# Optimization experiments

Hardware: AMD Instinct MI355X
Metric: run time of the kernel (lower is better)

## Reference

```python
import jax, jax.numpy as jnp
import numpy as np

VOCAB = 50257
EMBED = 256
NFREQ = 64
NRULES = 100
B, S = 4, 1024


def setup_inputs() -> dict:
    key = jax.random.key(0)
    ks = jax.random.split(key, 7)
    return {
        "token_ids": jax.random.randint(ks[0], (B, S), 0, VOCAB),
        "a_n": jax.random.normal(ks[1], (VOCAB, NFREQ), dtype=jnp.float32),
        "b_n": jax.random.normal(ks[2], (VOCAB, NFREQ), dtype=jnp.float32),
        "rule_transform": jax.random.normal(ks[3], (NRULES, EMBED, EMBED), dtype=jnp.float32),
        "token_rules": jax.random.randint(ks[4], (VOCAB,), 0, NRULES),
        "proj_w": jax.random.normal(ks[5], (EMBED, NFREQ), dtype=jnp.float32) * (1.0 / np.sqrt(NFREQ)),
        "proj_b": jax.random.normal(ks[6], (EMBED,), dtype=jnp.float32) * 0.01,
    }


def reference(token_ids, a_n, b_n, rule_transform, token_rules, proj_w, proj_b):
    vocab_size, nfreq = a_n.shape
    # fourier_freqs = linspace(1, F, F) -> [1..F]
    freqs = jnp.arange(1, nfreq + 1, dtype=jnp.float32)  # [F]
    x = token_ids.astype(jnp.float32)[..., None] / vocab_size  # [B,S,1]
    ang = (2.0 * jnp.pi) * freqs * x  # [B,S,F]
    # gather per-token fourier coefficients, fuse cos/sin combine
    fourier = a_n[token_ids] * jnp.cos(ang) + b_n[token_ids] * jnp.sin(ang)  # [B,S,F]
    base = jnp.einsum('bsf,df->bsd', fourier, proj_w) + proj_b  # [B,S,D]
    rule_idx = token_rules[token_ids]  # [B,S]
    rules = rule_transform[rule_idx]  # [B,S,D,D] gathered per token
    return jnp.einsum('bsd,bsde->bse', base, rules)  # [B,S,D]
```

## Files before the change

kernel.cpp:

```cpp
#include <hip/hip_runtime.h>
#include <math.h>

#define VOCAB   50257
#define EMBED   256
#define NFREQ   64
#define NRULES  100
#define NTOK    4096
#define CAP     256
#define CHUNK   16
#define NCHUNK  (CAP / CHUNK)

#define BASE_BYTES ((size_t)NTOK * EMBED * 4)
#define LIST_BYTES ((size_t)NRULES * CAP * 4)

__global__ __launch_bounds__(256) void prep_kernel(
    const float* __restrict__ proj_w,
    float*       __restrict__ wT,
    int*         __restrict__ counts)
{
    __shared__ float s_t[64 * 65];
    const int tid = threadIdx.x;
    const int b   = blockIdx.x;

    if (b == 0 && tid < NRULES) counts[tid] = 0;

    const float4* __restrict__ W4 =
        (const float4*)(proj_w + (size_t)b * 64 * NFREQ);
    #pragma unroll
    for (int i = 0; i < 4; ++i) {
        const int v = i * 256 + tid;
        const float4 w = W4[v];
        const int dl = v >> 4, f0 = (v & 15) * 4;
        s_t[dl * 65 + f0 + 0] = w.x;
        s_t[dl * 65 + f0 + 1] = w.y;
        s_t[dl * 65 + f0 + 2] = w.z;
        s_t[dl * 65 + f0 + 3] = w.w;
    }
    __syncthreads();
    #pragma unroll
    for (int j = 0; j < 16; ++j) {
        const int o = j * 256 + tid;
        const int f = o >> 6, c = o & 63;
        wT[f * EMBED + b * 64 + c] = s_t[c * 65 + f];
    }
}

__global__ __launch_bounds__(256) void fused_base_kernel(
    const int*   __restrict__ token_ids,
    const float* __restrict__ a_n,
    const float* __restrict__ b_n,
    const int*   __restrict__ token_rules,
    const float* __restrict__ wT,
    const float* __restrict__ proj_b,
    float*       __restrict__ base,
    int*         __restrict__ counts,
    int*         __restrict__ list)
{
    __shared__ float s_four[4][NFREQ];

    const int tid = threadIdx.x;
    const int tl  = tid >> 6;
    const int f   = tid & 63;
    const int tok_idx = blockIdx.x * 4 + tl;
    const int tok     = token_ids[tok_idx];

    const float x = (float)tok / (float)VOCAB;
    float sv, cv;
    sincosf(6.283185307179586f * x * (float)(f + 1), &sv, &cv);
    s_four[tl][f] = a_n[(size_t)tok * NFREQ + f] * cv
                  + b_n[(size_t)tok * NFREQ + f] * sv;

    if (f == 0) {
        const int rule = token_rules[tok];
        const int pos  = atomicAdd(&counts[rule], 1);
        if (pos < CAP) list[rule * CAP + pos] = tok_idx;
    }
    __syncthreads();

    const int   d    = tid;
    const float bias = proj_b[d];
    float a0 = bias, a1 = bias, a2 = bias, a3 = bias;

    #pragma unroll 4
    for (int q = 0; q < 16; ++q) {
        const float w0 = wT[(4 * q + 0) * EMBED + d];
        const float w1 = wT[(4 * q + 1) * EMBED + d];
        const float w2 = wT[(4 * q + 2) * EMBED + d];
        const float w3 = wT[(4 * q + 3) * EMBED + d];
        const float4 f0 = ((const float4*)s_four[0])[q];
        const float4 f1 = ((const float4*)s_four[1])[q];
        const float4 f2 = ((const float4*)s_four[2])[q];
        const float4 f3 = ((const float4*)s_four[3])[q];
        a0 += w0 * f0.x + w1 * f0.y + w2 * f0.z + w3 * f0.w;
        a1 += w0 * f1.x + w1 * f1.y + w2 * f1.z + w3 * f1.w;
        a2 += w0 * f2.x + w1 * f2.y + w2 * f2.z + w3 * f2.w;
        a3 += w0 * f3.x + w1 * f3.y + w2 * f3.z + w3 * f3.w;
    }
    base[(size_t)(blockIdx.x * 4 + 0) * EMBED + d] = a0;
    base[(size_t)(blockIdx.x * 4 + 1) * EMBED + d] = a1;
    base[(size_t)(blockIdx.x * 4 + 2) * EMBED + d] = a2;
    base[(size_t)(blockIdx.x * 4 + 3) * EMBED + d] = a3;
}

__global__ __launch_bounds__(512) void apply_kernel(
    const float* __restrict__ base,
    const float* __restrict__ rule_transform,
    const int*   __restrict__ counts,
    const int*   __restrict__ list,
    float*       __restrict__ out)
{
    __shared__ float s_mem[8192];

    const int rule = blockIdx.x;
    int cnt = counts[rule];
    if (cnt > CAP) cnt = CAP;
    const int t0 = blockIdx.y * CHUNK;
    if (t0 >= cnt) return;

    const int tid  = threadIdx.x;
    const int w8   = tid >> 6;
    const int ds   = w8 >> 1;
    const int eh   = w8 & 1;
    const int lane = tid & 63;

    #pragma unroll
    for (int i = 0; i < 8; ++i) {
        const int el = i * 512 + tid;
        int tt = t0 + (el >> 8);
        if (tt > cnt - 1) tt = cnt - 1;
        const int row = list[rule * CAP + tt];
        s_mem[el] = base[(size_t)row * EMBED + (el & 255)];
    }
    __syncthreads();

    const float2* __restrict__ T2 =
        (const float2*)(rule_transform + (size_t)rule * EMBED * EMBED);
    const int d0 = ds * 64;
    const int ec = eh * 64 + lane;

    float2 acc[CHUNK];
    #pragma unroll
    for (int t = 0; t < CHUNK; ++t) { acc[t].x = 0.f; acc[t].y = 0.f; }

    float2 tv[4], tvn[4];
    #pragma unroll
    for (int i = 0; i < 4; ++i)
        tv[i] = T2[(size_t)(d0 + i) * 128 + ec];

    for (int dq = 0; dq < 16; ++dq) {
        if (dq < 15) {
            #pragma unroll
            for (int i = 0; i < 4; ++i)
                tvn[i] = T2[(size_t)(d0 + dq * 4 + 4 + i) * 128 + ec];
        }
        #pragma unroll
        for (int t = 0; t < CHUNK; ++t) {
            const float4 b4 = *(const float4*)&s_mem[t * EMBED + d0 + dq * 4];
            acc[t].x += b4.x * tv[0].x + b4.y * tv[1].x + b4.z * tv[2].x + b4.w * tv[3].x;
            acc[t].y += b4.x * tv[0].y + b4.y * tv[1].y + b4.z * tv[2].y + b4.w * tv[3].y;
        }
        #pragma unroll
        for (int i = 0; i < 4; ++i) tv[i] = tvn[i];
    }

    __syncthreads();
    if (ds == 1 || ds == 3) {
        float2* dst = (float2*)(s_mem + ((ds >> 1) * 2 + eh) * 2048);
        #pragma unroll
        for (int t = 0; t < CHUNK; ++t) dst[t * 64 + lane] = acc[t];
    }
    __syncthreads();
    if (ds == 0 || ds == 2) {
        const float2* src = (const float2*)(s_mem + ((ds >> 1) * 2 + eh) * 2048);
        #pragma unroll
        for (int t = 0; t < CHUNK; ++t) {
            const float2 r = src[t * 64 + lane];
            acc[t].x += r.x; acc[t].y += r.y;
        }
    }
    __syncthreads();
    if (ds == 2) {
        float2* dst = (float2*)(s_mem + eh * 2048);
        #pragma unroll
        for (int t = 0; t < CHUNK; ++t) dst[t * 64 + lane] = acc[t];
    }
    __syncthreads();
    if (ds == 0) {
        const float2* src = (const float2*)(s_mem + eh * 2048);
        #pragma unroll
        for (int t = 0; t < CHUNK; ++t) {
            const float2 r = src[t * 64 + lane];
            acc[t].x += r.x; acc[t].y += r.y;
        }
        #pragma unroll
        for (int t = 0; t < CHUNK; ++t) {
            if (t0 + t < cnt) {
                const int row = list[rule * CAP + t0 + t];
                *(float2*)&out[(size_t)row * EMBED + eh * 128 + lane * 2] = acc[t];
            }
        }
    }
}

extern "C" void kernel_launch(void* const* d_in, const int* in_sizes, int n_in,
                              void* d_out, int out_size, void* d_ws, size_t ws_size,
                              hipStream_t stream) {
    const int*   token_ids      = (const int*)  d_in[0];
    const float* a_n            = (const float*)d_in[1];
    const float* b_n            = (const float*)d_in[2];
    const float* rule_transform = (const float*)d_in[3];
    const int*   token_rules    = (const int*)  d_in[4];
    const float* proj_w         = (const float*)d_in[5];
    const float* proj_b         = (const float*)d_in[6];
    float*       out            = (float*)d_out;

    float* base   = (float*)d_ws;
    int*   counts = (int*)((char*)d_ws + BASE_BYTES);
    int*   list   = (int*)((char*)d_ws + BASE_BYTES + 512);
    float* wT     = (float*)((char*)d_ws + BASE_BYTES + 512 + LIST_BYTES);

    prep_kernel<<<4, 256, 0, stream>>>(proj_w, wT, counts);
    fused_base_kernel<<<NTOK / 4, 256, 0, stream>>>(
        token_ids, a_n, b_n, token_rules, wT, proj_b, base, counts, list);
    apply_kernel<<<dim3(NRULES, NCHUNK), 512, 0, stream>>>(
        base, rule_transform, counts, list, out);
}
```

Before: 127.9 us.

## Tile apply kernel over output columns and loop over token tiles per rule

The apply kernel now splits each rule's work by output column tiles (64 columns per block, 4 blocks per rule) instead of by 16-token chunks, and each block loops over all of that rule's tokens in tiles of 48. Each thread covers the full 256-long reduction for one output column, so the cross-wave shared-memory reduction and its barriers are gone. Each rule matrix slice is now read once per token tile rather than once per 16-token chunk, which cuts rule_transform traffic. The trade-off is fewer blocks (400, all resident) with a serial loop over token tiles, a longer per-thread dependency chain, and less parallelism for rules with few tokens.

```diff
diff --git a/kernel.cpp b/kernel.cpp
--- a/kernel.cpp
+++ b/kernel.cpp
@@ -7,8 +7,9 @@
 #define NRULES  100
 #define NTOK    4096
 #define CAP     256
-#define CHUNK   16
-#define NCHUNK  (CAP / CHUNK)
+#define ETILE   64
+#define TTILE   48
+#define TPG     (TTILE / 4)
 
 #define BASE_BYTES ((size_t)NTOK * EMBED * 4)
 #define LIST_BYTES ((size_t)NRULES * CAP * 4)
@@ -102,101 +103,72 @@
     base[(size_t)(blockIdx.x * 4 + 3) * EMBED + d] = a3;
 }
 
-__global__ __launch_bounds__(512) void apply_kernel(
+__global__ __launch_bounds__(256) void apply_kernel(
     const float* __restrict__ base,
     const float* __restrict__ rule_transform,
     const int*   __restrict__ counts,
     const int*   __restrict__ list,
     float*       __restrict__ out)
 {
-    __shared__ float s_mem[8192];
+    __shared__ float s_base[TTILE * EMBED];
 
     const int rule = blockIdx.x;
     int cnt = counts[rule];
     if (cnt > CAP) cnt = CAP;
-    const int t0 = blockIdx.y * CHUNK;
-    if (t0 >= cnt) return;
+    if (cnt <= 0) return;
 
-    const int tid  = threadIdx.x;
-    const int w8   = tid >> 6;
-    const int ds   = w8 >> 1;
-    const int eh   = w8 & 1;
-    const int lane = tid & 63;
+    const int tid = threadIdx.x;
+    const int el  = tid & 63;
+    const int tg  = tid >> 6;
+    const int e   = blockIdx.y * ETILE + el;
 
-    #pragma unroll
-    for (int i = 0; i < 8; ++i) {
-        const int el = i * 512 + tid;
-        int tt = t0 + (el >> 8);
-        if (tt > cnt - 1) tt = cnt - 1;
-        const int row = list[rule * CAP + tt];
-        s_mem[el] = base[(size_t)row * EMBED + (el & 255)];
-    }
-    __syncthreads();
+    const float* __restrict__ T   = rule_transform + (size_t)rule * EMBED * EMBED;
+    const int*   __restrict__ lst = list + rule * CAP;
 
-    const float2* __restrict__ T2 =
-        (const float2*)(rule_transform + (size_t)rule * EMBED * EMBED);
-    const int d0 = ds * 64;
-    const int ec = eh * 64 + lane;
+    for (int t0 = 0; t0 < cnt; t0 += TTILE) {
+        __syncthreads();
+        for (int i = tid; i < TTILE * 64; i += 256) {
+            const int t = i >> 6, c = i & 63;
+            int tt = t0 + t;
+            if (tt > cnt - 1) tt = cnt - 1;
+            const int row = lst[tt];
+            ((float4*)s_base)[i] =
+                ((const float4*)(base + (size_t)row * EMBED))[c];
+        }
+        __syncthreads();
 
-    float2 acc[CHUNK];
-    #pragma unroll
-    for (int t = 0; t < CHUNK; ++t) { acc[t].x = 0.f; acc[t].y = 0.f; }
+        float acc[TPG];
+        #pragma unroll
+        for (int k = 0; k < TPG; ++k) acc[k] = 0.f;
 
-    float2 tv[4], tvn[4];
-    #pragma unroll
-    for (int i = 0; i < 4; ++i)
-        tv[i] = T2[(size_t)(d0 + i) * 128 + ec];
+        float tv[4], tvn[4];
+        #pragma unroll
+        for (int i = 0; i < 4; ++i)
+            tv[i] = T[(size_t)i * EMBED + e];
 
-    for (int dq = 0; dq < 16; ++dq) {
-        if (dq < 15) {
+        for (int dq = 0; dq < 64; ++dq) {
+            if (dq < 63) {
+                #pragma unroll
+                for (int i = 0; i < 4; ++i)
+                    tvn[i] = T[(size_t)((dq + 1) * 4 + i) * EMBED + e];
+            }
             #pragma unroll
-            for (int i = 0; i < 4; ++i)
-                tvn[i] = T2[(size_t)(d0 + dq * 4 + 4 + i) * 128 + ec];
+            for (int k = 0; k < TPG; ++k) {
+                const float4 b4 =
+                    *(const float4*)&s_base[(k * 4 + tg) * EMBED + dq * 4];
+                acc[k] += b4.x * tv[0] + b4.y * tv[1]
+                        + b4.z * tv[2] + b4.w * tv[3];
+            }
+            #pragma unroll
+            for (int i = 0; i < 4; ++i) tv[i] = tvn[i];
         }
+
         #pragma unroll
-        for (int t = 0; t < CHUNK; ++t) {
-            const float4 b4 = *(const float4*)&s_mem[t * EMBED + d0 + dq * 4];
-            acc[t].x += b4.x * tv[0].x + b4.y * tv[1].x + b4.z * tv[2].x + b4.w * tv[3].x;
-            acc[t].y += b4.x * tv[0].y + b4.y * tv[1].y + b4.z * tv[2].y + b4.w * tv[3].y;
-        }
-        #pragma unroll
-        for (int i = 0; i < 4; ++i) tv[i] = tvn[i];
-    }
-
-    __syncthreads();
-    if (ds == 1 || ds == 3) {
-        float2* dst = (float2*)(s_mem + ((ds >> 1) * 2 + eh) * 2048);
-        #pragma unroll
-        for (int t = 0; t < CHUNK; ++t) dst[t * 64 + lane] = acc[t];
-    }
-    __syncthreads();
-    if (ds == 0 || ds == 2) {
-        const float2* src = (const float2*)(s_mem + ((ds >> 1) * 2 + eh) * 2048);
-        #pragma unroll
-        for (int t = 0; t < CHUNK; ++t) {
-            const float2 r = src[t * 64 + lane];
-            acc[t].x += r.x; acc[t].y += r.y;
-        }
-    }
-    __syncthreads();
-    if (ds == 2) {
-        float2* dst = (float2*)(s_mem + eh * 2048);
-        #pragma unroll
-        for (int t = 0; t < CHUNK; ++t) dst[t * 64 + lane] = acc[t];
-    }
-    __syncthreads();
-    if (ds == 0) {
-        const float2* src = (const float2*)(s_mem + eh * 2048);
-        #pragma unroll
-        for (int t = 0; t < CHUNK; ++t) {
-            const float2 r = src[t * 64 + lane];
-            acc[t].x += r.x; acc[t].y += r.y;
-        }
-        #pragma unroll
-        for (int t = 0; t < CHUNK; ++t) {
-            if (t0 + t < cnt) {
-                const int row = list[rule * CAP + t0 + t];
-                *(float2*)&out[(size_t)row * EMBED + eh * 128 + lane * 2] = acc[t];
+        for (int k = 0; k < TPG; ++k) {
+            const int t = t0 + k * 4 + tg;
+            if (t < cnt) {
+                const int row = lst[t];
+                out[(size_t)row * EMBED + e] = acc[k];
             }
         }
     }
@@ -222,6 +194,6 @@
     prep_kernel<<<4, 256, 0, stream>>>(proj_w, wT, counts);
     fused_base_kernel<<<NTOK / 4, 256, 0, stream>>>(
         token_ids, a_n, b_n, token_rules, wT, proj_b, base, counts, list);
-    apply_kernel<<<dim3(NRULES, NCHUNK), 512, 0, stream>>>(
+    apply_kernel<<<dim3(NRULES, EMBED / ETILE), 256, 0, stream>>>(
         base, rule_transform, counts, list, out);
 }
```

Result: slower. 158.9 us (+24.2%).

## Split apply kernel output columns across blocks to double grid parallelism

Applied to the files above, without the earlier changes.

The apply kernel now splits the 256 output columns into two halves on a new grid dimension. Each thread computes one column as a scalar instead of a float2 pair, and shared memory is halved. This doubles the block count and lowers per-thread register pressure, aiming for better occupancy. In exchange each block reloads the base rows for its chunk, and rule-transform loads become scalar instead of float2.

```diff
diff --git a/kernel.cpp b/kernel.cpp
--- a/kernel.cpp
+++ b/kernel.cpp
@@ -109,55 +109,59 @@
     const int*   __restrict__ list,
     float*       __restrict__ out)
 {
-    __shared__ float s_mem[8192];
+    __shared__ float s_mem[4096];
 
     const int rule = blockIdx.x;
+    const int eh   = blockIdx.y;
     int cnt = counts[rule];
     if (cnt > CAP) cnt = CAP;
-    const int t0 = blockIdx.y * CHUNK;
+    const int t0 = blockIdx.z * CHUNK;
     if (t0 >= cnt) return;
 
     const int tid  = threadIdx.x;
     const int w8   = tid >> 6;
     const int ds   = w8 >> 1;
-    const int eh   = w8 & 1;
+    const int es   = w8 & 1;
     const int lane = tid & 63;
-
-    #pragma unroll
-    for (int i = 0; i < 8; ++i) {
-        const int el = i * 512 + tid;
-        int tt = t0 + (el >> 8);
+    const int ec   = eh * 128 + es * 64 + lane;
+
+    const int* __restrict__ lst = list + rule * CAP;
+
+    #pragma unroll
+    for (int i = 0; i < 2; ++i) {
+        const int v = i * 512 + tid;
+        int tt = t0 + (v >> 6);
         if (tt > cnt - 1) tt = cnt - 1;
-        const int row = list[rule * CAP + tt];
-        s_mem[el] = base[(size_t)row * EMBED + (el & 255)];
-    }
-    __syncthreads();
-
-    const float2* __restrict__ T2 =
-        (const float2*)(rule_transform + (size_t)rule * EMBED * EMBED);
+        const int row = lst[tt];
+        ((float4*)s_mem)[v] =
+            ((const float4*)(base + (size_t)row * EMBED))[v & 63];
+    }
+    __syncthreads();
+
+    const float* __restrict__ T =
+        rule_transform + (size_t)rule * EMBED * EMBED;
     const int d0 = ds * 64;
-    const int ec = eh * 64 + lane;
-
-    float2 acc[CHUNK];
-    #pragma unroll
-    for (int t = 0; t < CHUNK; ++t) { acc[t].x = 0.f; acc[t].y = 0.f; }
-
-    float2 tv[4], tvn[4];
+
+    float acc[CHUNK];
+    #pragma unroll
+    for (int t = 0; t < CHUNK; ++t) acc[t] = 0.f;
+
+    float tv[4], tvn[4];
     #pragma unroll
     for (int i = 0; i < 4; ++i)
-        tv[i] = T2[(size_t)(d0 + i) * 128 + ec];
+        tv[i] = T[(size_t)(d0 + i) * EMBED + ec];
 
     for (int dq = 0; dq < 16; ++dq) {
         if (dq < 15) {
             #pragma unroll
             for (int i = 0; i < 4; ++i)
-                tvn[i] = T2[(size_t)(d0 + dq * 4 + 4 + i) * 128 + ec];
+                tvn[i] = T[(size_t)(d0 + dq * 4 + 4 + i) * EMBED + ec];
         }
         #pragma unroll
         for (int t = 0; t < CHUNK; ++t) {
             const float4 b4 = *(const float4*)&s_mem[t * EMBED + d0 + dq * 4];
-            acc[t].x += b4.x * tv[0].x + b4.y * tv[1].x + b4.z * tv[2].x + b4.w * tv[3].x;
-            acc[t].y += b4.x * tv[0].y + b4.y * tv[1].y + b4.z * tv[2].y + b4.w * tv[3].y;
+            acc[t] += b4.x * tv[0] + b4.y * tv[1]
+                    + b4.z * tv[2] + b4.w * tv[3];
         }
         #pragma unroll
         for (int i = 0; i < 4; ++i) tv[i] = tvn[i];
@@ -165,38 +169,32 @@
 
     __syncthreads();
     if (ds == 1 || ds == 3) {
-        float2* dst = (float2*)(s_mem + ((ds >> 1) * 2 + eh) * 2048);
+        float* dst = s_mem + ((ds >> 1) * 2 + es) * 1024;
         #pragma unroll
         for (int t = 0; t < CHUNK; ++t) dst[t * 64 + lane] = acc[t];
     }
     __syncthreads();
     if (ds == 0 || ds == 2) {
-        const float2* src = (const float2*)(s_mem + ((ds >> 1) * 2 + eh) * 2048);
-        #pragma unroll
-        for (int t = 0; t < CHUNK; ++t) {
-            const float2 r = src[t * 64 + lane];
-            acc[t].x += r.x; acc[t].y += r.y;
-        }
+        const float* src = s_mem + ((ds >> 1) * 2 + es) * 1024;
+        #pragma unroll
+        for (int t = 0; t < CHUNK; ++t) acc[t] += src[t * 64 + lane];
     }
     __syncthreads();
     if (ds == 2) {
-        float2* dst = (float2*)(s_mem + eh * 2048);
+        float* dst = s_mem + es * 1024;
         #pragma unroll
         for (int t = 0; t < CHUNK; ++t) dst[t * 64 + lane] = acc[t];
     }
     __syncthreads();
     if (ds == 0) {
-        const float2* src = (const float2*)(s_mem + eh * 2048);
-        #pragma unroll
-        for (int t = 0; t < CHUNK; ++t) {
-            const float2 r = src[t * 64 + lane];
-            acc[t].x += r.x; acc[t].y += r.y;
-        }
+        const float* src = s_mem + es * 1024;
+        #pragma unroll
+        for (int t = 0; t < CHUNK; ++t) acc[t] += src[t * 64 + lane];
         #pragma unroll
         for (int t = 0; t < CHUNK; ++t) {
             if (t0 + t < cnt) {
-                const int row = list[rule * CAP + t0 + t];
-                *(float2*)&out[(size_t)row * EMBED + eh * 128 + lane * 2] = acc[t];
+                const int row = lst[t0 + t];
+                out[(size_t)row * EMBED + ec] = acc[t];
             }
         }
     }
@@ -210,8 +208,8 @@
     const float* b_n            = (const float*)d_in[2];
     const float* rule_transform = (const float*)d_in[3];
     const int*   token_rules    = (const int*)  d_in[4];
+    const float* proj_b         = (const float*)d_in[6];
     const float* proj_w         = (const float*)d_in[5];
-    const float* proj_b         = (const float*)d_in[6];
     float*       out            = (float*)d_out;
 
     float* base   = (float*)d_ws;
@@ -222,6 +220,6 @@
     prep_kernel<<<4, 256, 0, stream>>>(proj_w, wT, counts);
     fused_base_kernel<<<NTOK / 4, 256, 0, stream>>>(
         token_ids, a_n, b_n, token_rules, wT, proj_b, base, counts, list);
-    apply_kernel<<<dim3(NRULES, NCHUNK), 512, 0, stream>>>(
+    apply_kernel<<<dim3(NRULES, 2, NCHUNK), 512, 0, stream>>>(
         base, rule_transform, counts, list, out);
 }
```

New measurement: 133.6 us. 1.04x slower.
